# Optimization experiments

Hardware: AMD Instinct MI355X
Metric: run time of the kernel (lower is better)

## Reference

```python
import jax, jax.numpy as jnp
import numpy as np

HID, H, KV, S, B = 2048, 32, 8, 2048, 2
D = HID // H           # head_dim = 64
G = H // KV            # query heads per kv head = 4


def setup_inputs() -> dict:
    key = jax.random.key(0)
    ks = jax.random.split(key, 10)
    sc = 0.02
    kv_dim = HID * KV // H  # 512
    return {
        "x": jax.random.normal(ks[0], (B, S, HID), jnp.float32),
        "attention_mask": jnp.zeros((B, S), jnp.float32),
        "Wq": jax.random.normal(ks[1], (HID, HID), jnp.float32) * sc,
        "bq": jnp.zeros((HID,), jnp.float32),
        "Wk": jax.random.normal(ks[2], (kv_dim, HID), jnp.float32) * sc,
        "bk": jnp.zeros((kv_dim,), jnp.float32),
        "Wv": jax.random.normal(ks[3], (kv_dim, HID), jnp.float32) * sc,
        "bv": jnp.zeros((kv_dim,), jnp.float32),
        "Wo": jax.random.normal(ks[4], (HID, HID), jnp.float32) * sc,
        "bo": jnp.zeros((HID,), jnp.float32),
    }


def reference(x, attention_mask, Wq, bq, Wk, bk, Wv, bv, Wo, bo):
    Bx, Sx, _ = x.shape
    # projections (torch Linear: x @ W.T + b)
    q = x @ Wq.T + bq                                  # [B,S,HID]
    k = x @ Wk.T + bk                                  # [B,S,KV*D]
    v = x @ Wv.T + bv
    # split heads: [B,S,H,D] -> [B,H,S,D]; then group q: [B,KV,G,S,D]
    q = q.reshape(Bx, Sx, H, D).transpose(0, 2, 1, 3).reshape(Bx, KV, G, Sx, D)
    k = k.reshape(Bx, Sx, KV, D).transpose(0, 2, 1, 3)  # [B,KV,S,D]
    v = v.reshape(Bx, Sx, KV, D).transpose(0, 2, 1, 3)
    scale = 1.0 / jnp.sqrt(jnp.float32(D))
    scores = jnp.einsum('bkgsd,bktd->bkgst', q, k) * scale  # [B,KV,G,S,S]
    scores = scores + attention_mask[:, None, None, None, :]
    attn = jax.nn.softmax(scores, axis=-1)
    out = jnp.einsum('bkgst,bktd->bkgsd', attn, v)          # [B,KV,G,S,D]
    out = out.reshape(Bx, H, Sx, D).transpose(0, 2, 1, 3).reshape(Bx, Sx, HID)
    return out @ Wo.T + bo
```

## Files before the change

kernel.cpp:

```cpp
#include <hip/hip_runtime.h>
#include <hip/hip_bf16.h>
#include <stdint.h>

typedef __hip_bfloat16 bf16;
typedef __attribute__((ext_vector_type(8))) short bf16x8;
typedef __attribute__((ext_vector_type(4))) float f32x4;
typedef __attribute__((ext_vector_type(16))) float f32x16;
typedef __attribute__((ext_vector_type(4))) int i32x4;
typedef __attribute__((ext_vector_type(2))) int i32x2;

#define B_   2
#define S_   2048
#define HID_ 2048
#define H_   32
#define KV_  8
#define D_   64
#define NT_  (S_ / 64)
#define LOG2E 1.4426950408889634f

__device__ __forceinline__ void gload_lds16(const void* g, void* l) {
  __builtin_amdgcn_global_load_lds(
      (const __attribute__((address_space(1))) uint32_t*)g,
      (__attribute__((address_space(3))) uint32_t*)l, 16, 0, 0);
}
__device__ __forceinline__ float fexp2(float x) { return __builtin_amdgcn_exp2f(x); }

__device__ __forceinline__ uint32_t cvtpk_bf16(float lo, float hi) {
  uint32_t r;
  asm("v_cvt_pk_bf16_f32 %0, %1, %2" : "=v"(r) : "v"(lo), "v"(hi));
  return r;
}
__device__ __forceinline__ void plane32_swap(uint32_t& a, uint32_t& b) {
  i32x2 r = __builtin_amdgcn_permlane32_swap((int)a, (int)b, false, false);
  a = (uint32_t)r[0]; b = (uint32_t)r[1];
}

__global__ __launch_bounds__(256) void cvt_f32_bf16(
    const float* __restrict__ s, bf16* __restrict__ d, int n4) {
  int i = blockIdx.x * blockDim.x + threadIdx.x;
  const int stride = gridDim.x * blockDim.x;
  for (; i < n4; i += stride) {
    float4 v = ((const float4*)s)[i];
    bf16 t[4];
    t[0] = __float2bfloat16(v.x);
    t[1] = __float2bfloat16(v.y);
    t[2] = __float2bfloat16(v.z);
    t[3] = __float2bfloat16(v.w);
    *reinterpret_cast<uint64_t*>(d + 4 * (size_t)i) = *reinterpret_cast<uint64_t*>(t);
  }
}

__global__ __launch_bounds__(256) void mask_prep(
    const float* __restrict__ m, float* __restrict__ o, int n) {
  int i = blockIdx.x * blockDim.x + threadIdx.x;
  if (i < n) o[i] = m[i] * LOG2E;
}

__global__ __launch_bounds__(256, 2) void gemm_qkv(
    const bf16* __restrict__ A,
    const bf16* __restrict__ Wqp, const bf16* __restrict__ Wkp, const bf16* __restrict__ Wvp,
    const float* __restrict__ bqp, const float* __restrict__ bkp, const float* __restrict__ bvp,
    bf16* __restrict__ Cq, bf16* __restrict__ Ck, bf16* __restrict__ Cv) {
  const int bn_all = blockIdx.y;
  const bf16* W; const float* bias; bf16* C; int Hn; int bn;
  if (bn_all < 16)      { W = Wqp; bias = bqp; C = Cq; Hn = H_;  bn = bn_all; }
  else if (bn_all < 20) { W = Wkp; bias = bkp; C = Ck; Hn = KV_; bn = bn_all - 16; }
  else                  { W = Wvp; bias = bvp; C = Cv; Hn = KV_; bn = bn_all - 20; }
  const float oscale = (bn_all < 16) ? (0.125f * LOG2E) : 1.0f;

  __shared__ __align__(16) bf16 As[128 * 64];
  __shared__ __align__(16) bf16 Bs[128 * 64];
  const int tid = threadIdx.x;
  const int lane = tid & 63, wid = tid >> 6;
  const int wr = wid >> 1, wc = wid & 1;
  const int bm = blockIdx.x;
  const int K = HID_;

  f32x4 acc[4][4] = {};

  for (int k0 = 0; k0 < K; k0 += 64) {
    __syncthreads();
#pragma unroll
    for (int c = 0; c < 4; ++c) {
      const int r = c * 32 + wid * 8 + (lane >> 3);
      const int gcolb = ((lane & 7) * 16) ^ ((r & 7) << 4);
      gload_lds16(A + (size_t)(bm * 128 + r) * K + k0 + (gcolb >> 1),
                  &As[(c * 32 + wid * 8) * 64]);
      gload_lds16(W + (size_t)(bn * 128 + r) * K + k0 + (gcolb >> 1),
                  &Bs[(c * 32 + wid * 8) * 64]);
    }
    __syncthreads();
#pragma unroll
    for (int ks = 0; ks < 2; ++ks) {
      bf16x8 af[4], bfr[4];
#pragma unroll
      for (int i = 0; i < 4; ++i) {
        const int ra = wr * 64 + i * 16 + (lane & 15);
        const int ka = (ks * 64 + ((lane >> 4) << 4)) ^ ((ra & 7) << 4);
        af[i] = *(const bf16x8*)((const char*)As + ra * 128 + ka);
        const int rb = wc * 64 + i * 16 + (lane & 15);
        const int kb = (ks * 64 + ((lane >> 4) << 4)) ^ ((rb & 7) << 4);
        bfr[i] = *(const bf16x8*)((const char*)Bs + rb * 128 + kb);
      }
      __builtin_amdgcn_s_setprio(1);
#pragma unroll
      for (int i = 0; i < 4; ++i)
#pragma unroll
        for (int j = 0; j < 4; ++j)
          acc[i][j] = __builtin_amdgcn_mfma_f32_16x16x32_bf16(af[i], bfr[j], acc[i][j], 0, 0, 0);
      __builtin_amdgcn_s_setprio(0);
    }
  }

#pragma unroll
  for (int j = 0; j < 4; ++j) {
    const int n = bn * 128 + wc * 64 + j * 16 + (lane & 15);
    const float bv = bias[n];
#pragma unroll
    for (int i = 0; i < 4; ++i) {
      const int mb = bm * 128 + wr * 64 + i * 16 + ((lane >> 4) << 2);
#pragma unroll
      for (int e = 0; e < 4; ++e) {
        const int m = mb + e;
        const float v = (acc[i][j][e] + bv) * oscale;
        const int b = m >> 11, s = m & (S_ - 1);
        const int h = n >> 6, d = n & 63;
        C[(((size_t)b * Hn + h) * S_ + s) * 64 + d] = __float2bfloat16(v);
      }
    }
  }
}

__global__ __launch_bounds__(256, 2) void gemm_out(
    const bf16* __restrict__ A, const bf16* __restrict__ W,
    const float* __restrict__ bias, float* __restrict__ C) {
  __shared__ __align__(16) bf16 As[128 * 64];
  __shared__ __align__(16) bf16 Bs[128 * 64];
  const int tid = threadIdx.x;
  const int lane = tid & 63, wid = tid >> 6;
  const int wr = wid >> 1, wc = wid & 1;
  const int bm = blockIdx.x, bn = blockIdx.y;
  const int K = HID_, N = HID_;

  f32x4 acc[4][4] = {};

  for (int k0 = 0; k0 < K; k0 += 64) {
    __syncthreads();
#pragma unroll
    for (int c = 0; c < 4; ++c) {
      const int r = c * 32 + wid * 8 + (lane >> 3);
      const int gcolb = ((lane & 7) * 16) ^ ((r & 7) << 4);
      gload_lds16(A + (size_t)(bm * 128 + r) * K + k0 + (gcolb >> 1),
                  &As[(c * 32 + wid * 8) * 64]);
      gload_lds16(W + (size_t)(bn * 128 + r) * K + k0 + (gcolb >> 1),
                  &Bs[(c * 32 + wid * 8) * 64]);
    }
    __syncthreads();
#pragma unroll
    for (int ks = 0; ks < 2; ++ks) {
      bf16x8 af[4], bfr[4];
#pragma unroll
      for (int i = 0; i < 4; ++i) {
        const int ra = wr * 64 + i * 16 + (lane & 15);
        const int ka = (ks * 64 + ((lane >> 4) << 4)) ^ ((ra & 7) << 4);
        af[i] = *(const bf16x8*)((const char*)As + ra * 128 + ka);
        const int rb = wc * 64 + i * 16 + (lane & 15);
        const int kb = (ks * 64 + ((lane >> 4) << 4)) ^ ((rb & 7) << 4);
        bfr[i] = *(const bf16x8*)((const char*)Bs + rb * 128 + kb);
      }
      __builtin_amdgcn_s_setprio(1);
#pragma unroll
      for (int i = 0; i < 4; ++i)
#pragma unroll
        for (int j = 0; j < 4; ++j)
          acc[i][j] = __builtin_amdgcn_mfma_f32_16x16x32_bf16(af[i], bfr[j], acc[i][j], 0, 0, 0);
      __builtin_amdgcn_s_setprio(0);
    }
  }

#pragma unroll
  for (int j = 0; j < 4; ++j) {
    const int n = bn * 128 + wc * 64 + j * 16 + (lane & 15);
    const float bv = bias[n];
#pragma unroll
    for (int i = 0; i < 4; ++i) {
      const int mb = bm * 128 + wr * 64 + i * 16 + ((lane >> 4) << 2);
#pragma unroll
      for (int e = 0; e < 4; ++e) {
        C[(size_t)(mb + e) * N + n] = acc[i][j][e] + bv;
      }
    }
  }
}

__global__ __launch_bounds__(256, 4) void attn_fwd(
    const bf16* __restrict__ qb, const bf16* __restrict__ kb,
    const bf16* __restrict__ vb, const float* __restrict__ maskL,
    bf16* __restrict__ ob) {
  const int qtile = blockIdx.x;
  const int headid = blockIdx.y;
  const int b = headid >> 5, h = headid & (H_ - 1);
  const int kv = h >> 2;
  const int tid = threadIdx.x, lane = tid & 63, wid = tid >> 6;
  const int l31 = lane & 31, hi = lane >> 5;

  __shared__ __align__(16) bf16 Ks[2][64 * 64];
  __shared__ __align__(16) bf16 VTs[2][64 * 64];
  __shared__ float lsm[4][32];

  const bf16* qh = qb + ((size_t)(b * H_ + h) * S_) * D_;
  const bf16* kh = kb + ((size_t)(b * KV_ + kv) * S_) * D_;
  const bf16* vh = vb + ((size_t)(b * KV_ + kv) * S_) * D_;
  const float* mrow = maskL + (size_t)b * S_;

  const int qrow = qtile * 128 + wid * 32 + l31;
  bf16x8 qf[4];
#pragma unroll
  for (int ks = 0; ks < 4; ++ks)
    qf[ks] = *(const bf16x8*)(qh + (size_t)qrow * D_ + ks * 16 + hi * 8);

  float lp = 0.f;
  f32x16 o[2] = {};

#pragma unroll
  for (int c = 0; c < 2; ++c) {
    const int r = c * 32 + wid * 8 + (lane >> 3);
    const int gcolb = ((lane & 7) * 16) ^ ((r & 7) << 4);
    gload_lds16(kh + (size_t)r * D_ + (gcolb >> 1), &Ks[0][(c * 32 + wid * 8) * 64]);
  }
  bf16x8 vn0 = *(const bf16x8*)(vh + (size_t)lane * D_ + wid * 16);
  bf16x8 vn1 = *(const bf16x8*)(vh + (size_t)lane * D_ + wid * 16 + 8);
  {
    const int key2 = lane * 2;
#pragma unroll
    for (int j2 = 0; j2 < 8; ++j2) {
      const int d0 = wid * 16 + j2;
      *(short*)((char*)&VTs[0][0] + d0 * 128 + (key2 ^ ((d0 & 7) << 4))) = vn0[j2];
      const int d1 = d0 + 8;
      *(short*)((char*)&VTs[0][0] + d1 * 128 + (key2 ^ ((d1 & 7) << 4))) = vn1[j2];
    }
  }
  __syncthreads();

  for (int t = 0; t < NT_; ++t) {
    const int cur = t & 1, nxt = cur ^ 1;

    if (t < NT_ - 1) {
#pragma unroll
      for (int c = 0; c < 2; ++c) {
        const int r = c * 32 + wid * 8 + (lane >> 3);
        const int gcolb = ((lane & 7) * 16) ^ ((r & 7) << 4);
        gload_lds16(kh + ((size_t)(t + 1) * 64 + r) * D_ + (gcolb >> 1),
                    &Ks[nxt][(c * 32 + wid * 8) * 64]);
      }
      vn0 = *(const bf16x8*)(vh + ((size_t)(t + 1) * 64 + lane) * D_ + wid * 16);
      vn1 = *(const bf16x8*)(vh + ((size_t)(t + 1) * 64 + lane) * D_ + wid * 16 + 8);
    }

    f32x16 s[2];
#pragma unroll
    for (int kbv = 0; kbv < 2; ++kbv) {
#pragma unroll
      for (int rq = 0; rq < 4; ++rq) {
        const f32x4 m4 = *(const f32x4*)(mrow + t * 64 + kbv * 32 + rq * 8 + 4 * hi);
#pragma unroll
        for (int e = 0; e < 4; ++e) s[kbv][rq * 4 + e] = m4[e];
      }
    }
#pragma unroll
    for (int kbv = 0; kbv < 2; ++kbv) {
      __builtin_amdgcn_s_setprio(1);
#pragma unroll
      for (int ks = 0; ks < 4; ++ks) {
        const int rk = kbv * 32 + l31;
        const int kbyte = (ks * 32 + hi * 16) ^ ((rk & 7) << 4);
        bf16x8 kf = *(const bf16x8*)((const char*)&Ks[cur][0] + rk * 128 + kbyte);
        s[kbv] = __builtin_amdgcn_mfma_f32_32x32x16_bf16(kf, qf[ks], s[kbv], 0, 0, 0);
      }
      __builtin_amdgcn_s_setprio(0);
    }

    float2 ps2 = make_float2(0.f, 0.f);
#pragma unroll
    for (int kbv = 0; kbv < 2; ++kbv)
#pragma unroll
      for (int r8 = 0; r8 < 8; ++r8) {
        const float pa_ = fexp2(s[kbv][2 * r8]);
        const float pb_ = fexp2(s[kbv][2 * r8 + 1]);
        s[kbv][2 * r8] = pa_;
        s[kbv][2 * r8 + 1] = pb_;
        ps2.x += pa_;
        ps2.y += pb_;
      }
    lp += ps2.x + ps2.y;

    bf16x8 pa[2][2];
#pragma unroll
    for (int kbv = 0; kbv < 2; ++kbv) {
      uint32_t a0 = cvtpk_bf16(s[kbv][0], s[kbv][1]);
      uint32_t b0 = cvtpk_bf16(s[kbv][4], s[kbv][5]);
      plane32_swap(a0, b0);
      uint32_t a1 = cvtpk_bf16(s[kbv][2], s[kbv][3]);
      uint32_t b1 = cvtpk_bf16(s[kbv][6], s[kbv][7]);
      plane32_swap(a1, b1);
      i32x4 t0; t0[0] = (int)a0; t0[1] = (int)a1; t0[2] = (int)b0; t0[3] = (int)b1;
      pa[kbv][0] = __builtin_bit_cast(bf16x8, t0);
      uint32_t a2 = cvtpk_bf16(s[kbv][8], s[kbv][9]);
      uint32_t b2 = cvtpk_bf16(s[kbv][12], s[kbv][13]);
      plane32_swap(a2, b2);
      uint32_t a3 = cvtpk_bf16(s[kbv][10], s[kbv][11]);
      uint32_t b3 = cvtpk_bf16(s[kbv][14], s[kbv][15]);
      plane32_swap(a3, b3);
      i32x4 t1; t1[0] = (int)a2; t1[1] = (int)a3; t1[2] = (int)b2; t1[3] = (int)b3;
      pa[kbv][1] = __builtin_bit_cast(bf16x8, t1);
    }

#pragma unroll
    for (int db = 0; db < 2; ++db) {
      __builtin_amdgcn_s_setprio(1);
#pragma unroll
      for (int kbv = 0; kbv < 2; ++kbv)
#pragma unroll
        for (int ks2 = 0; ks2 < 2; ++ks2) {
          const int rd = db * 32 + l31;
          const int vbyte = (kbv * 64 + ks2 * 32 + hi * 16) ^ ((rd & 7) << 4);
          bf16x8 vf = *(const bf16x8*)((const char*)&VTs[cur][0] + rd * 128 + vbyte);
          o[db] = __builtin_amdgcn_mfma_f32_32x32x16_bf16(pa[kbv][ks2], vf, o[db], 0, 0, 0);
        }
      __builtin_amdgcn_s_setprio(0);
    }

    __syncthreads();
    if (t < NT_ - 1) {
      const int key2 = lane * 2;
#pragma unroll
      for (int j2 = 0; j2 < 8; ++j2) {
        const int d0 = wid * 16 + j2;
        *(short*)((char*)&VTs[nxt][0] + d0 * 128 + (key2 ^ ((d0 & 7) << 4))) = vn0[j2];
        const int d1 = d0 + 8;
        *(short*)((char*)&VTs[nxt][0] + d1 * 128 + (key2 ^ ((d1 & 7) << 4))) = vn1[j2];
      }
    }
    __syncthreads();
  }

  {
    uint32_t la = __float_as_uint(lp), lb = la;
    plane32_swap(la, lb);
    const float lsum = __uint_as_float(la) + __uint_as_float(lb);
    lsm[wid][l31] = lsum;
  }
  __syncthreads();
#pragma unroll
  for (int rq = 0; rq < 4; ++rq) {
    const f32x4 l4 = *(const f32x4*)&lsm[wid][rq * 8 + 4 * hi];
#pragma unroll
    for (int e2 = 0; e2 < 4; ++e2) {
      const float inv = 1.0f / l4[e2];
      const int q_out = e2 + 8 * rq + 4 * hi;
      const int srow = qtile * 128 + wid * 32 + q_out;
#pragma unroll
      for (int db = 0; db < 2; ++db) {
        const float val = o[db][rq * 4 + e2] * inv;
        ob[((size_t)b * S_ + srow) * HID_ + h * 64 + db * 32 + l31] = __float2bfloat16(val);
      }
    }
  }
}

extern "C" void kernel_launch(void* const* d_in, const int* in_sizes, int n_in,
                              void* d_out, int out_size, void* d_ws, size_t ws_size,
                              hipStream_t stream) {
  (void)in_sizes; (void)n_in; (void)out_size; (void)ws_size;
  const float* x  = (const float*)d_in[0];
  const float* am = (const float*)d_in[1];
  const float* Wq = (const float*)d_in[2];
  const float* bq = (const float*)d_in[3];
  const float* Wk = (const float*)d_in[4];
  const float* bk = (const float*)d_in[5];
  const float* Wv = (const float*)d_in[6];
  const float* bv = (const float*)d_in[7];
  const float* Wo = (const float*)d_in[8];
  const float* bo = (const float*)d_in[9];
  float* out = (float*)d_out;

  const size_t XE  = (size_t)B_ * S_ * HID_;
  const size_t WQE = (size_t)HID_ * HID_;
  const size_t WKE = (size_t)(KV_ * D_) * HID_;
  const size_t QE  = (size_t)B_ * H_ * S_ * D_;
  const size_t KE  = (size_t)B_ * KV_ * S_ * D_;

  bf16* xb  = (bf16*)d_ws;
  bf16* wqb = xb + XE;
  bf16* wkb = wqb + WQE;
  bf16* wvb = wkb + WKE;
  bf16* wob = wvb + WKE;
  bf16* qbuf = wob + WQE;
  bf16* kbuf = qbuf + QE;
  bf16* vbuf = kbuf + KE;
  bf16* abuf = vbuf + KE;
  float* maskL = (float*)(abuf + XE);

  dim3 blk(256);
  cvt_f32_bf16<<<2048, blk, 0, stream>>>(x,  xb,  (int)(XE / 4));
  cvt_f32_bf16<<<2048, blk, 0, stream>>>(Wq, wqb, (int)(WQE / 4));
  cvt_f32_bf16<<<1024, blk, 0, stream>>>(Wk, wkb, (int)(WKE / 4));
  cvt_f32_bf16<<<1024, blk, 0, stream>>>(Wv, wvb, (int)(WKE / 4));
  cvt_f32_bf16<<<2048, blk, 0, stream>>>(Wo, wob, (int)(WQE / 4));
  mask_prep<<<(B_ * S_ + 255) / 256, blk, 0, stream>>>(am, maskL, B_ * S_);

  const int M = B_ * S_;
  gemm_qkv<<<dim3(M / 128, 24), blk, 0, stream>>>(xb, wqb, wkb, wvb, bq, bk, bv,
                                                  qbuf, kbuf, vbuf);
  attn_fwd<<<dim3(S_ / 128, B_ * H_), blk, 0, stream>>>(qbuf, kbuf, vbuf, maskL, abuf);
  gemm_out<<<dim3(M / 128, HID_ / 128), blk, 0, stream>>>(abuf, wob, bo, out);
}
```

Measured before the change: 209.6 us.

## Write V transposed from QKV GEMM and remap blocks for XCD locality

The QKV projection epilogue now writes V in a [B,KV,D,S] transposed layout, so the attention kernel can load V^T tiles straight into LDS with async global-to-LDS loads. This removes the per-tile register transposition and the extra barrier in the attention loop. All three kernels also remap block IDs so that consecutive logical tiles land on the same XCD (stride by grid/8), which is meant to improve L2 reuse of shared K/V and weight tiles. The cost is a strided V store in the GEMM epilogue, and the remap assumes the grid size divides by 8.

```diff
diff --git a/kernel.cpp b/kernel.cpp
--- a/kernel.cpp
+++ b/kernel.cpp
@@ -61,11 +61,16 @@
     const bf16* __restrict__ Wqp, const bf16* __restrict__ Wkp, const bf16* __restrict__ Wvp,
     const float* __restrict__ bqp, const float* __restrict__ bkp, const float* __restrict__ bvp,
     bf16* __restrict__ Cq, bf16* __restrict__ Ck, bf16* __restrict__ Cv) {
-  const int bn_all = blockIdx.y;
-  const bf16* W; const float* bias; bf16* C; int Hn; int bn;
-  if (bn_all < 16)      { W = Wqp; bias = bqp; C = Cq; Hn = H_;  bn = bn_all; }
-  else if (bn_all < 20) { W = Wkp; bias = bkp; C = Ck; Hn = KV_; bn = bn_all - 16; }
-  else                  { W = Wvp; bias = bvp; C = Cv; Hn = KV_; bn = bn_all - 20; }
+  const int lid0 = blockIdx.y * gridDim.x + blockIdx.x;
+  const int q8 = (int)(gridDim.x * gridDim.y) >> 3;
+  const int lid = (lid0 & 7) * q8 + (lid0 >> 3);
+  const int bm = lid & 31;
+  const int bn_all = lid >> 5;
+
+  const bf16* W; const float* bias; int bn;
+  if (bn_all < 16)      { W = Wqp; bias = bqp; bn = bn_all; }
+  else if (bn_all < 20) { W = Wkp; bias = bkp; bn = bn_all - 16; }
+  else                  { W = Wvp; bias = bvp; bn = bn_all - 20; }
   const float oscale = (bn_all < 16) ? (0.125f * LOG2E) : 1.0f;
 
   __shared__ __align__(16) bf16 As[128 * 64];
@@ -73,7 +78,6 @@
   const int tid = threadIdx.x;
   const int lane = tid & 63, wid = tid >> 6;
   const int wr = wid >> 1, wc = wid & 1;
-  const int bm = blockIdx.x;
   const int K = HID_;
 
   f32x4 acc[4][4] = {};
@@ -112,20 +116,42 @@
     }
   }
 
-#pragma unroll
-  for (int j = 0; j < 4; ++j) {
-    const int n = bn * 128 + wc * 64 + j * 16 + (lane & 15);
-    const float bv = bias[n];
-#pragma unroll
-    for (int i = 0; i < 4; ++i) {
-      const int mb = bm * 128 + wr * 64 + i * 16 + ((lane >> 4) << 2);
-#pragma unroll
-      for (int e = 0; e < 4; ++e) {
-        const int m = mb + e;
-        const float v = (acc[i][j][e] + bv) * oscale;
-        const int b = m >> 11, s = m & (S_ - 1);
-        const int h = n >> 6, d = n & 63;
-        C[(((size_t)b * Hn + h) * S_ + s) * 64 + d] = __float2bfloat16(v);
+  if (bn_all < 20) {
+    const int Hn = (bn_all < 16) ? H_ : KV_;
+    bf16* C = (bn_all < 16) ? Cq : Ck;
+#pragma unroll
+    for (int j = 0; j < 4; ++j) {
+      const int n = bn * 128 + wc * 64 + j * 16 + (lane & 15);
+      const float bv = bias[n];
+#pragma unroll
+      for (int i = 0; i < 4; ++i) {
+        const int mb = bm * 128 + wr * 64 + i * 16 + ((lane >> 4) << 2);
+#pragma unroll
+        for (int e = 0; e < 4; ++e) {
+          const int m = mb + e;
+          const float v = (acc[i][j][e] + bv) * oscale;
+          const int b = m >> 11, s = m & (S_ - 1);
+          const int h = n >> 6, d = n & 63;
+          C[(((size_t)b * Hn + h) * S_ + s) * 64 + d] = __float2bfloat16(v);
+        }
+      }
+    }
+  } else {
+#pragma unroll
+    for (int j = 0; j < 4; ++j) {
+      const int n = bn * 128 + wc * 64 + j * 16 + (lane & 15);
+      const int kvh = n >> 6, d = n & 63;
+      const float bv = bias[n];
+#pragma unroll
+      for (int i = 0; i < 4; ++i) {
+        const int m0 = bm * 128 + wr * 64 + i * 16 + ((lane >> 4) << 2);
+        const int b = m0 >> 11, s0 = m0 & (S_ - 1);
+        bf16 t4[4];
+#pragma unroll
+        for (int e = 0; e < 4; ++e) t4[e] = __float2bfloat16(acc[i][j][e] + bv);
+        *reinterpret_cast<uint64_t*>(
+            Cv + (((size_t)b * KV_ + kvh) * D_ + d) * S_ + s0) =
+            *reinterpret_cast<uint64_t*>(t4);
       }
     }
   }
@@ -134,12 +160,17 @@
 __global__ __launch_bounds__(256, 2) void gemm_out(
     const bf16* __restrict__ A, const bf16* __restrict__ W,
     const float* __restrict__ bias, float* __restrict__ C) {
+  const int lid0 = blockIdx.y * gridDim.x + blockIdx.x;
+  const int q8 = (int)(gridDim.x * gridDim.y) >> 3;
+  const int lid = (lid0 & 7) * q8 + (lid0 >> 3);
+  const int bm = lid & 31;
+  const int bn = lid >> 5;
+
   __shared__ __align__(16) bf16 As[128 * 64];
   __shared__ __align__(16) bf16 Bs[128 * 64];
   const int tid = threadIdx.x;
   const int lane = tid & 63, wid = tid >> 6;
   const int wr = wid >> 1, wc = wid & 1;
-  const int bm = blockIdx.x, bn = blockIdx.y;
   const int K = HID_, N = HID_;
 
   f32x4 acc[4][4] = {};
@@ -195,10 +226,13 @@
 
 __global__ __launch_bounds__(256, 4) void attn_fwd(
     const bf16* __restrict__ qb, const bf16* __restrict__ kb,
-    const bf16* __restrict__ vb, const float* __restrict__ maskL,
+    const bf16* __restrict__ vtb, const float* __restrict__ maskL,
     bf16* __restrict__ ob) {
-  const int qtile = blockIdx.x;
-  const int headid = blockIdx.y;
+  const int lid0 = blockIdx.y * gridDim.x + blockIdx.x;
+  const int q8 = (int)(gridDim.x * gridDim.y) >> 3;
+  const int lid = (lid0 & 7) * q8 + (lid0 >> 3);
+  const int qtile = lid & 15;
+  const int headid = lid >> 4;
   const int b = headid >> 5, h = headid & (H_ - 1);
   const int kv = h >> 2;
   const int tid = threadIdx.x, lane = tid & 63, wid = tid >> 6;
@@ -210,7 +244,7 @@
 
   const bf16* qh = qb + ((size_t)(b * H_ + h) * S_) * D_;
   const bf16* kh = kb + ((size_t)(b * KV_ + kv) * S_) * D_;
-  const bf16* vh = vb + ((size_t)(b * KV_ + kv) * S_) * D_;
+  const bf16* vth = vtb + (size_t)(b * KV_ + kv) * D_ * S_;
   const float* mrow = maskL + (size_t)b * S_;
 
   const int qrow = qtile * 128 + wid * 32 + l31;
@@ -227,18 +261,7 @@
     const int r = c * 32 + wid * 8 + (lane >> 3);
     const int gcolb = ((lane & 7) * 16) ^ ((r & 7) << 4);
     gload_lds16(kh + (size_t)r * D_ + (gcolb >> 1), &Ks[0][(c * 32 + wid * 8) * 64]);
-  }
-  bf16x8 vn0 = *(const bf16x8*)(vh + (size_t)lane * D_ + wid * 16);
-  bf16x8 vn1 = *(const bf16x8*)(vh + (size_t)lane * D_ + wid * 16 + 8);
-  {
-    const int key2 = lane * 2;
-#pragma unroll
-    for (int j2 = 0; j2 < 8; ++j2) {
-      const int d0 = wid * 16 + j2;
-      *(short*)((char*)&VTs[0][0] + d0 * 128 + (key2 ^ ((d0 & 7) << 4))) = vn0[j2];
-      const int d1 = d0 + 8;
-      *(short*)((char*)&VTs[0][0] + d1 * 128 + (key2 ^ ((d1 & 7) << 4))) = vn1[j2];
-    }
+    gload_lds16(vth + (size_t)r * S_ + (gcolb >> 1), &VTs[0][(c * 32 + wid * 8) * 64]);
   }
   __syncthreads();
 
@@ -252,9 +275,9 @@
         const int gcolb = ((lane & 7) * 16) ^ ((r & 7) << 4);
         gload_lds16(kh + ((size_t)(t + 1) * 64 + r) * D_ + (gcolb >> 1),
                     &Ks[nxt][(c * 32 + wid * 8) * 64]);
-      }
-      vn0 = *(const bf16x8*)(vh + ((size_t)(t + 1) * 64 + lane) * D_ + wid * 16);
-      vn1 = *(const bf16x8*)(vh + ((size_t)(t + 1) * 64 + lane) * D_ + wid * 16 + 8);
+        gload_lds16(vth + (size_t)r * S_ + (t + 1) * 64 + (gcolb >> 1),
+                    &VTs[nxt][(c * 32 + wid * 8) * 64]);
+      }
     }
 
     f32x16 s[2];
@@ -331,17 +354,6 @@
     }
 
     __syncthreads();
-    if (t < NT_ - 1) {
-      const int key2 = lane * 2;
-#pragma unroll
-      for (int j2 = 0; j2 < 8; ++j2) {
-        const int d0 = wid * 16 + j2;
-        *(short*)((char*)&VTs[nxt][0] + d0 * 128 + (key2 ^ ((d0 & 7) << 4))) = vn0[j2];
-        const int d1 = d0 + 8;
-        *(short*)((char*)&VTs[nxt][0] + d1 * 128 + (key2 ^ ((d1 & 7) << 4))) = vn1[j2];
-      }
-    }
-    __syncthreads();
   }
 
   {
@@ -397,8 +409,8 @@
   bf16* wob = wvb + WKE;
   bf16* qbuf = wob + WQE;
   bf16* kbuf = qbuf + QE;
-  bf16* vbuf = kbuf + KE;
-  bf16* abuf = vbuf + KE;
+  bf16* vtbuf = kbuf + KE;
+  bf16* abuf = vtbuf + KE;
   float* maskL = (float*)(abuf + XE);
 
   dim3 blk(256);
@@ -411,7 +423,7 @@
 
   const int M = B_ * S_;
   gemm_qkv<<<dim3(M / 128, 24), blk, 0, stream>>>(xb, wqb, wkb, wvb, bq, bk, bv,
-                                                  qbuf, kbuf, vbuf);
-  attn_fwd<<<dim3(S_ / 128, B_ * H_), blk, 0, stream>>>(qbuf, kbuf, vbuf, maskL, abuf);
+                                                  qbuf, kbuf, vtbuf);
+  attn_fwd<<<dim3(S_ / 128, B_ * H_), blk, 0, stream>>>(qbuf, kbuf, vtbuf, maskL, abuf);
   gemm_out<<<dim3(M / 128, HID_ / 128), blk, 0, stream>>>(abuf, wob, bo, out);
 }
```

Result: faster. 202.5 us (-3.4%).
